# Optimization experiments

Measured on AMD Instinct MI355X. Metric: run time of the kernel, lower is better.

## Reference

```python
import jax, jax.numpy as jnp
import numpy as np

B, L, D, H = 2, 2048, 1024, 16
HD = D // H


def setup_inputs() -> dict:
    key = jax.random.key(0)
    ks = jax.random.split(key, 12)
    s = 1.0 / np.sqrt(D)
    inp = {
        "q": jax.random.normal(ks[0], (B, L, D), jnp.float32),
        "k": jax.random.normal(ks[1], (B, L, D), jnp.float32),
        "v": jax.random.normal(ks[2], (B, L, D), jnp.float32),
        "mask": jnp.zeros((B, L), dtype=bool),  # True = masked out
        "Wq": jax.random.normal(ks[3], (D, D), jnp.float32) * s,
        "bq": jnp.zeros((D,), jnp.float32),
        "Wk": jax.random.normal(ks[4], (D, D), jnp.float32) * s,
        "bk": jnp.zeros((D,), jnp.float32),
        "Wv": jax.random.normal(ks[5], (D, D), jnp.float32) * s,
        "bv": jnp.zeros((D,), jnp.float32),
        "Wo": jax.random.normal(ks[6], (D, D), jnp.float32) * s,
        "bo": jnp.zeros((D,), jnp.float32),
    }
    return inp


def reference(q, k, v, mask, Wq, bq, Wk, bk, Wv, bv, Wo, bo):
    # linear projections (torch Linear: x @ W.T + b), split into heads: [B,H,L,HD]
    def proj(x, W, b):
        y = jnp.einsum('bld,ed->ble', x, W) + b
        return y.reshape(x.shape[0], x.shape[1], H, HD).transpose(0, 2, 1, 3)

    Q = proj(q, Wq, bq)
    K = proj(k, Wk, bk)
    V = proj(v, Wv, bv)

    scale = 1.0 / np.sqrt(HD).astype(np.float32)
    scores = jnp.einsum('bhqd,bhkd->bhqk', Q, K) * scale  # [B,H,Lq,Lk]
    # mask [B,Lk] -> broadcast over heads and query positions
    scores = jnp.where(mask[:, None, None, :], -jnp.inf, scores)
    attn = jax.nn.softmax(scores, axis=-1)
    out = jnp.einsum('bhqk,bhkd->bhqd', attn, V)  # [B,H,Lq,HD]
    out = out.transpose(0, 2, 1, 3).reshape(q.shape[0], q.shape[1], D)
    return jnp.einsum('bld,ed->ble', out, Wo) + bo
```

## Files before the change

### kernel.cpp

```cpp
#include <hip/hip_runtime.h>

#define LSEQ 2048
#define DMODEL 1024
#define NHEAD 16
#define HDIM 64

typedef __attribute__((ext_vector_type(8))) short bf16x8;
typedef __attribute__((ext_vector_type(4))) float f32x4;
typedef __attribute__((ext_vector_type(16))) float f32x16;
typedef unsigned int u32;
typedef unsigned short u16;
typedef unsigned long long u64;

static __device__ __forceinline__ u16 f2bf(float x) {
    return (u16)((__builtin_bit_cast(u32, x) + 0x8000u) >> 16);
}

static __device__ __forceinline__ u32 f2bf_pk(float hi, float lo) {
    u32 a = __builtin_bit_cast(u32, hi) + 0x8000u;
    u32 b = __builtin_bit_cast(u32, lo) + 0x8000u;
#if __has_builtin(__builtin_amdgcn_perm)
    return __builtin_amdgcn_perm(a, b, 0x07060302u);
#else
    return (a & 0xFFFF0000u) | (b >> 16);
#endif
}

static __device__ __forceinline__ float bf2f(short s) {
    return __builtin_bit_cast(float, (u32)((u16)s) << 16);
}

static __device__ __forceinline__ float fast_exp2(float x) {
#if __has_builtin(__builtin_amdgcn_exp2f)
    return __builtin_amdgcn_exp2f(x);
#else
    return __expf(x * 0.6931471805599453f);
#endif
}

static __device__ __forceinline__ void gll16(const void* g, void* l) {
    __builtin_amdgcn_global_load_lds(
        (const __attribute__((address_space(1))) u32*)g,
        (__attribute__((address_space(3))) u32*)l, 16, 0, 0);
}

template <int N>
static __device__ __forceinline__ void vwait() {
    asm volatile("s_waitcnt vmcnt(%0)" :: "n"(N) : "memory");
}

__global__ __launch_bounds__(256) void conv_all(
    const float* __restrict__ q, const float* __restrict__ k, const float* __restrict__ v,
    const float* __restrict__ w0, const float* __restrict__ w1,
    const float* __restrict__ w2, const float* __restrict__ w3,
    u16* __restrict__ Qf, u16* __restrict__ Kf, u16* __restrict__ Vf,
    u16* __restrict__ o0, u16* __restrict__ o1, u16* __restrict__ o2,
    u16* __restrict__ o3) {
    const int bid = blockIdx.x;
    const float* s; u16* d; int off;
    if (bid < 12288) {
        const int z = bid >> 12;
        off = bid & 4095;
        if (z == 0)      { s = q; d = Qf; }
        else if (z == 1) { s = k; d = Kf; }
        else             { s = v; d = Vf; }
    } else {
        const int t = bid - 12288;
        const int z = t >> 10;
        off = t & 1023;
        if (z == 0)      { s = w0; d = o0; }
        else if (z == 1) { s = w1; d = o1; }
        else if (z == 2) { s = w2; d = o2; }
        else             { s = w3; d = o3; }
    }
    const int i = (off * 256 + threadIdx.x) * 4;
    float4 x = *(const float4*)(s + i);
    uint2 r;
    r.x = f2bf_pk(x.y, x.x);
    r.y = f2bf_pk(x.w, x.z);
    *(uint2*)(d + i) = r;
}

template <int OUT_MODE, int BN>
__device__ __forceinline__ void mfma_gemm(u16* __restrict__ sm,
                                          const u16* __restrict__ Xb,
                                          const u16* __restrict__ Wb,
                                          const float* __restrict__ bias,
                                          void* __restrict__ Yv, float scale) {
    constexpr int NB = BN / 32;
    constexpr int LPT = (BN == 128) ? 4 : 3;
    constexpr int ASZ = 4096;
    constexpr int BSZ = BN * 32;
    constexpr int NT = DMODEL / 32;
    u16* As = sm;
    u16* Bs = sm + 3 * ASZ;

    const int tid = threadIdx.x;
    const int wave = tid >> 6, lane = tid & 63;
    const int l16 = lane & 15, quad = lane >> 4;
    const int wm = (wave >> 1) * 64, wn = (wave & 1) * (BN / 2);
    const int m0 = blockIdx.x * 128, n0 = blockIdx.y * BN;

    const u16* Xr = Xb + (size_t)(m0 + (tid >> 2)) * DMODEL + (tid & 3) * 8;
    const u16* Wr = Wb + (size_t)(n0 + (tid >> 2)) * DMODEL + (tid & 3) * 8;
    const int t8 = tid * 8;

    auto stage = [&](int kt, int slot) {
        const int k0 = kt * 32;
        u16* Ab = As + slot * ASZ;
        u16* Bb = Bs + slot * BSZ;
        gll16(Xr + k0, Ab + t8);
        gll16(Xr + (size_t)64 * DMODEL + k0, Ab + 2048 + t8);
        gll16(Wr + k0, Bb + t8);
        if (BN == 128)
            gll16(Wr + (size_t)64 * DMODEL + k0, Bb + 2048 + t8);
    };

    f32x4 acc[4][NB];
    #pragma unroll
    for (int i = 0; i < 4; ++i)
        #pragma unroll
        for (int j = 0; j < NB; ++j)
            #pragma unroll
            for (int r = 0; r < 4; ++r) acc[i][j][r] = 0.0f;

    auto compute = [&](int kt) {
        const u16* Ac = As + (kt % 3) * ASZ;
        const u16* Bc = Bs + (kt % 3) * BSZ;
        bf16x8 af[4], bf[NB];
        #pragma unroll
        for (int mb = 0; mb < 4; ++mb)
            af[mb] = *(const bf16x8*)(Ac + (wm + mb * 16 + l16) * 32 + quad * 8);
        #pragma unroll
        for (int nb = 0; nb < NB; ++nb)
            bf[nb] = *(const bf16x8*)(Bc + (wn + nb * 16 + l16) * 32 + quad * 8);
        #pragma unroll
        for (int mb = 0; mb < 4; ++mb)
            #pragma unroll
            for (int nb = 0; nb < NB; ++nb)
                acc[mb][nb] = __builtin_amdgcn_mfma_f32_16x16x32_bf16(
                    af[mb], bf[nb], acc[mb][nb], 0, 0, 0);
    };

    stage(0, 0);
    stage(1, 1);

    #pragma unroll 1
    for (int kt = 0; kt < NT - 1; ++kt) {
        vwait<LPT>();
        __builtin_amdgcn_s_barrier();
        if (kt + 2 < NT) stage(kt + 2, (kt + 2) % 3);
        compute(kt);
    }
    vwait<0>();
    __builtin_amdgcn_s_barrier();
    compute(NT - 1);

    #pragma unroll
    for (int nb = 0; nb < NB; ++nb) {
        const int n = n0 + wn + nb * 16 + l16;
        const float bn = bias[n];
        #pragma unroll
        for (int mb = 0; mb < 4; ++mb) {
            const int mb0 = m0 + wm + mb * 16 + quad * 4;
            if (OUT_MODE == 2) {
                u16* Y = (u16*)Yv;
                uint2 rr;
                rr.x = f2bf_pk((acc[mb][nb][1] + bn) * scale, (acc[mb][nb][0] + bn) * scale);
                rr.y = f2bf_pk((acc[mb][nb][3] + bn) * scale, (acc[mb][nb][2] + bn) * scale);
                const int bb = mb0 >> 11, l = mb0 & 2047;
                const int h = n >> 6, hd = n & 63;
                *(uint2*)(Y + ((size_t)((bb * NHEAD + h) * HDIM) + hd) * LSEQ + l) = rr;
            } else {
                #pragma unroll
                for (int r = 0; r < 4; ++r) {
                    const int m = mb0 + r;
                    const float val = (acc[mb][nb][r] + bn) * scale;
                    if (OUT_MODE == 0) {
                        u16* Y = (u16*)Yv;
                        const int bb = m >> 11, l = m & 2047;
                        const int h = n >> 6, hd = n & 63;
                        Y[(((size_t)(bb * NHEAD + h) * LSEQ + l) * HDIM) + hd] = f2bf(val);
                    } else {
                        float* Y = (float*)Yv;
                        Y[(size_t)m * DMODEL + n] = val;
                    }
                }
            }
        }
    }
}

#define QSCALE (0.125f * 1.4426950408889634f)

__global__ __launch_bounds__(256) void qkv_gemm(
    const u16* __restrict__ Qf, const u16* __restrict__ Kf, const u16* __restrict__ Vf,
    const u16* __restrict__ Wqb, const u16* __restrict__ Wkb, const u16* __restrict__ Wvb,
    const float* __restrict__ bq, const float* __restrict__ bk, const float* __restrict__ bv,
    u16* __restrict__ Qp, u16* __restrict__ Kp, u16* __restrict__ Vtp) {
    __shared__ alignas(16) u16 sm[24576];
    if (blockIdx.z == 0)      mfma_gemm<0, 128>(sm, Qf, Wqb, bq, (void*)Qp, QSCALE);
    else if (blockIdx.z == 1) mfma_gemm<0, 128>(sm, Kf, Wkb, bk, (void*)Kp, 1.0f);
    else                      mfma_gemm<2, 128>(sm, Vf, Wvb, bv, (void*)Vtp, 1.0f);
}

__global__ __launch_bounds__(256) void out_gemm(
    const u16* __restrict__ AOb, const u16* __restrict__ Wob,
    const float* __restrict__ bo, float* __restrict__ out) {
    __shared__ alignas(16) u16 sm[18432];
    mfma_gemm<1, 64>(sm, AOb, Wob, bo, (void*)out, 1.0f);
}

#define KT 128
#define NTILE (LSEQ / KT)
#define HTILE (NTILE / 2)

__global__ __launch_bounds__(512, 4) void attn_mfma(
    const u16* __restrict__ Qp, const u16* __restrict__ Kp,
    const u16* __restrict__ Vtp, const unsigned char* __restrict__ mask,
    u16* __restrict__ P0, u16* __restrict__ P1, float* __restrict__ lbuf) {
    __shared__ alignas(16) u16 smem[32768];

    const int tid = threadIdx.x;
    const int wave = tid >> 6;
    const int lane = tid & 63;
    const int l32 = lane & 31;
    const int half = lane >> 5;
    const int bh = blockIdx.x;
    const int b = bh >> 4;
    const int h = bh & 15;
    const int q0 = blockIdx.y * 256;
    const int qw = q0 + wave * 32;
    const int z = blockIdx.z;
    const int kt0 = z * HTILE, kt1 = kt0 + HTILE;

    u16* Pz = z ? P1 : P0;
    float* lb = lbuf + z * (32 * LSEQ);

    const u16* Qg = Qp + ((size_t)bh * LSEQ + qw) * HDIM;
    const u16* Kg = Kp + (size_t)bh * LSEQ * HDIM;
    const u16* Vtg = Vtp + (size_t)bh * HDIM * LSEQ;
    const unsigned char* mg = mask + (size_t)b * LSEQ;

    bf16x8 qf[4];
    #pragma unroll
    for (int dc = 0; dc < 4; ++dc)
        qf[dc] = *(const bf16x8*)(Qg + (size_t)l32 * HDIM + dc * 16 + half * 8);

    f32x16 o0 = {}, o1 = {};
    float lsum = 0.0f;

    auto stageK = [&](int ktile, int slot) {
        const int k0 = ktile * KT;
        u16* Kb = smem + slot * 8192;
        #pragma unroll
        for (int j = 0; j < 2; ++j) {
            const int cid = j * 512 + tid;
            const int key = cid >> 3, pc = cid & 7, c = pc ^ (key & 7);
            gll16(Kg + (size_t)(k0 + key) * HDIM + c * 8, Kb + cid * 8);
        }
    };
    auto stageV = [&](int ktile, int slot) {
        const int k0 = ktile * KT;
        u16* Vb = smem + 16384 + slot * 8192;
        #pragma unroll
        for (int j = 0; j < 2; ++j) {
            const int cid = j * 512 + tid;
            const int d = cid >> 4, pc = cid & 15, c = pc ^ (d & 15);
            gll16(Vtg + (size_t)d * LSEQ + k0 + c * 8, Vb + cid * 8);
        }
    };

    stageK(kt0, kt0 & 1); stageV(kt0, kt0 & 1);

    const u64* mg8 = (const u64*)mg;
    const u64 mm = mg8[lane] | mg8[lane + 64] | mg8[lane + 128] | mg8[lane + 192];
    const bool mask_any = __any((int)(mm != 0ULL));

    __syncthreads();

    for (int kt = kt0; kt < kt1; ++kt) {
        if (kt + 1 < kt1) {
            stageK(kt + 1, (kt + 1) & 1);
            stageV(kt + 1, (kt + 1) & 1);
        }
        const u16* Kb = smem + (kt & 1) * 8192;
        const u16* Vb = smem + 16384 + (kt & 1) * 8192;

        #pragma unroll 1
        for (int kb = 0; kb < 4; ++kb) {
            f32x16 st = {};
            #pragma unroll
            for (int dc = 0; dc < 4; ++dc) {
                const int key = kb * 32 + l32;
                const int phys = (dc * 2 + half) ^ (key & 7);
                bf16x8 kf = *(const bf16x8*)(Kb + key * 64 + phys * 8);
                st = __builtin_amdgcn_mfma_f32_32x32x16_bf16(kf, qf[dc], st, 0, 0, 0);
            }

            if (mask_any) {
                const int k0 = kt * KT;
                const int mb0 = mg[k0 + lane];
                const int mb1 = mg[k0 + 64 + lane];
                const float b0f = mb0 ? -1e30f : 0.0f;
                const float b1f = mb1 ? -1e30f : 0.0f;
                #pragma unroll
                for (int r = 0; r < 16; ++r) {
                    const int key = kb * 32 + (r & 3) + 8 * (r >> 2) + 4 * half;
                    const float bv = __shfl((kb < 2) ? b0f : b1f, key & 63, 64);
                    st[r] += bv;
                }
            }

            u32 pk[8];
            float lk0 = 0.0f, lk1 = 0.0f;
            #pragma unroll
            for (int w = 0; w < 8; ++w) {
                const float plo = fast_exp2(st[2 * w]);
                const float phi = fast_exp2(st[2 * w + 1]);
                lk0 += plo; lk1 += phi;
                pk[w] = f2bf_pk(phi, plo);
            }
            lsum += lk0 + lk1;

            #pragma unroll
            for (int wb = 0; wb < 8; wb += 4) {
#if __has_builtin(__builtin_amdgcn_permlane32_swap)
                auto r02 = __builtin_amdgcn_permlane32_swap(
                    (int)pk[wb],     (int)pk[wb + 2], false, false);
                auto r13 = __builtin_amdgcn_permlane32_swap(
                    (int)pk[wb + 1], (int)pk[wb + 3], false, false);
                pk[wb]     = (u32)r02[0]; pk[wb + 2] = (u32)r02[1];
                pk[wb + 1] = (u32)r13[0]; pk[wb + 3] = (u32)r13[1];
#else
                const u32 ta = half ? pk[wb] : pk[wb + 2];
                const u32 tb = half ? pk[wb + 1] : pk[wb + 3];
                const u32 xa = __shfl_xor((int)ta, 32, 64);
                const u32 xb = __shfl_xor((int)tb, 32, 64);
                pk[wb]     = half ? xa : pk[wb];
                pk[wb + 1] = half ? xb : pk[wb + 1];
                pk[wb + 2] = half ? pk[wb + 2] : xa;
                pk[wb + 3] = half ? pk[wb + 3] : xb;
#endif
            }

            #pragma unroll
            for (int cc = 0; cc < 2; ++cc) {
                const int c = 2 * kb + cc;
                bf16x8 pb = __builtin_bit_cast(bf16x8, *(uint4*)&pk[4 * cc]);
                {
                    const int d = l32;
                    const int phys = (c * 2 + half) ^ (d & 15);
                    bf16x8 va = *(const bf16x8*)(Vb + d * 128 + phys * 8);
                    o0 = __builtin_amdgcn_mfma_f32_32x32x16_bf16(va, pb, o0, 0, 0, 0);
                }
                {
                    const int d = 32 + l32;
                    const int phys = (c * 2 + half) ^ (d & 15);
                    bf16x8 va = *(const bf16x8*)(Vb + d * 128 + phys * 8);
                    o1 = __builtin_amdgcn_mfma_f32_32x32x16_bf16(va, pb, o1, 0, 0, 0);
                }
            }
        }

        __syncthreads();
    }

    const float l_tot = lsum + __shfl_xor(lsum, 32, 64);
    if (!half) lb[bh * LSEQ + qw + l32] = l_tot;
    __syncthreads();
    u16* T = smem;
    #pragma unroll
    for (int nb = 0; nb < 2; ++nb)
        #pragma unroll
        for (int rp = 0; rp < 8; ++rp) {
            const int r = rp * 2;
            const int d = nb * 32 + (r & 3) + 8 * (r >> 2) + 4 * half;
            const float vlo = (nb ? o1[r] : o0[r]);
            const float vhi = (nb ? o1[r + 1] : o0[r + 1]);
            *(u32*)(T + (wave * 32 + l32) * 72 + d) = f2bf_pk(vhi, vlo);
        }
    __syncthreads();
    #pragma unroll
    for (int i = 0; i < 4; ++i) {
        const int cid = i * 512 + tid;
        const int row = cid >> 3, ch = cid & 7;
        bf16x8 val = *(const bf16x8*)(T + row * 72 + ch * 8);
        *(bf16x8*)(Pz + ((size_t)(b * LSEQ + q0 + row) * DMODEL) + h * HDIM + ch * 8) = val;
    }
}

__global__ __launch_bounds__(256) void combine(
    const u16* __restrict__ P0, const u16* __restrict__ P1,
    const float* __restrict__ lbuf, u16* __restrict__ AOb) {
    const int c = (blockIdx.x * 256 + threadIdx.x) * 8;
    const int bl = c >> 10;
    const int k = c & 1023;
    const int h = k >> 6;
    const int b = bl >> 11, l = bl & 2047;
    const int li = ((b << 4) + h) * LSEQ + l;
    const float inv = 1.0f / (lbuf[li] + lbuf[32 * LSEQ + li]);
    bf16x8 x0 = *(const bf16x8*)(P0 + c);
    bf16x8 x1 = *(const bf16x8*)(P1 + c);
    u32 r[4];
    #pragma unroll
    for (int j = 0; j < 4; ++j) {
        const float lo = (bf2f(x0[2 * j]) + bf2f(x1[2 * j])) * inv;
        const float hi = (bf2f(x0[2 * j + 1]) + bf2f(x1[2 * j + 1])) * inv;
        r[j] = f2bf_pk(hi, lo);
    }
    *(uint4*)(AOb + c) = *(uint4*)r;
}

extern "C" void kernel_launch(void* const* d_in, const int* in_sizes, int n_in,
                              void* d_out, int out_size, void* d_ws, size_t ws_size,
                              hipStream_t stream) {
    (void)in_sizes; (void)n_in; (void)out_size; (void)ws_size;
    const float* q  = (const float*)d_in[0];
    const float* k  = (const float*)d_in[1];
    const float* v  = (const float*)d_in[2];
    const unsigned char* mask = (const unsigned char*)d_in[3];
    const float* Wq = (const float*)d_in[4];
    const float* bq = (const float*)d_in[5];
    const float* Wk = (const float*)d_in[6];
    const float* bk = (const float*)d_in[7];
    const float* Wv = (const float*)d_in[8];
    const float* bv = (const float*)d_in[9];
    const float* Wo = (const float*)d_in[10];
    const float* bo = (const float*)d_in[11];
    float* out = (float*)d_out;

    u16* ws16 = (u16*)d_ws;
    const size_t M4 = (size_t)4 * 1024 * 1024;
    const size_t M1 = (size_t)1024 * 1024;
    u16* Qf  = ws16;
    u16* Kf  = ws16 + M4;
    u16* Vf  = ws16 + 2 * M4;
    u16* Qp  = ws16 + 3 * M4;
    u16* Kp  = ws16 + 4 * M4;
    u16* Vtp = ws16 + 5 * M4;
    u16* AOb = ws16 + 6 * M4;
    u16* Wqb = ws16 + 7 * M4;
    u16* Wkb = ws16 + 7 * M4 + M1;
    u16* Wvb = ws16 + 7 * M4 + 2 * M1;
    u16* Wob = ws16 + 7 * M4 + 3 * M1;

    u16* P0 = Qf;
    u16* P1 = Kf;
    float* lbuf = (float*)Vf;

    conv_all<<<dim3(16384), 256, 0, stream>>>(q, k, v, Wq, Wk, Wv, Wo,
                                              Qf, Kf, Vf, Wqb, Wkb, Wvb, Wob);
    qkv_gemm<<<dim3(32, 8, 3), 256, 0, stream>>>(Qf, Kf, Vf, Wqb, Wkb, Wvb,
                                                 bq, bk, bv, Qp, Kp, Vtp);
    attn_mfma<<<dim3(32, 8, 2), 512, 0, stream>>>(Qp, Kp, Vtp, mask, P0, P1, lbuf);
    combine<<<dim3(2048), 256, 0, stream>>>(P0, P1, lbuf, AOb);
    out_gemm<<<dim3(32, 16), 256, 0, stream>>>(AOb, Wob, bo, out);
}
```

Measured before the change: 216.2 us.

## Drop split-K attention and combine kernel; read V directly from global

Removes the two-way key split across blockIdx.z, so each attention block walks all key tiles and normalizes its own output. The separate combine kernel and its partial buffers go away. V is no longer staged in LDS and is loaded straight from global memory inside the PV loop, which shrinks shared memory. Launch bounds drop from 4 to 2 blocks per SM. The cost is half as many attention blocks, 256 in place of 512, which lowers parallelism. The uncoalesced, unpipelined global V loads may also stall the MFMA loop.

```diff
diff --git a/kernel.cpp b/kernel.cpp
--- a/kernel.cpp
+++ b/kernel.cpp
@@ -24,10 +24,6 @@
 #else
     return (a & 0xFFFF0000u) | (b >> 16);
 #endif
-}
-
-static __device__ __forceinline__ float bf2f(short s) {
-    return __builtin_bit_cast(float, (u32)((u16)s) << 16);
 }
 
 static __device__ __forceinline__ float fast_exp2(float x) {
@@ -213,13 +209,12 @@
 
 #define KT 128
 #define NTILE (LSEQ / KT)
-#define HTILE (NTILE / 2)
-
-__global__ __launch_bounds__(512, 4) void attn_mfma(
+
+__global__ __launch_bounds__(512, 2) void attn_mfma(
     const u16* __restrict__ Qp, const u16* __restrict__ Kp,
     const u16* __restrict__ Vtp, const unsigned char* __restrict__ mask,
-    u16* __restrict__ P0, u16* __restrict__ P1, float* __restrict__ lbuf) {
-    __shared__ alignas(16) u16 smem[32768];
+    u16* __restrict__ AOb) {
+    __shared__ alignas(16) u16 smem[18432];
 
     const int tid = threadIdx.x;
     const int wave = tid >> 6;
@@ -231,11 +226,6 @@
     const int h = bh & 15;
     const int q0 = blockIdx.y * 256;
     const int qw = q0 + wave * 32;
-    const int z = blockIdx.z;
-    const int kt0 = z * HTILE, kt1 = kt0 + HTILE;
-
-    u16* Pz = z ? P1 : P0;
-    float* lb = lbuf + z * (32 * LSEQ);
 
     const u16* Qg = Qp + ((size_t)bh * LSEQ + qw) * HDIM;
     const u16* Kg = Kp + (size_t)bh * LSEQ * HDIM;
@@ -260,18 +250,8 @@
             gll16(Kg + (size_t)(k0 + key) * HDIM + c * 8, Kb + cid * 8);
         }
     };
-    auto stageV = [&](int ktile, int slot) {
-        const int k0 = ktile * KT;
-        u16* Vb = smem + 16384 + slot * 8192;
-        #pragma unroll
-        for (int j = 0; j < 2; ++j) {
-            const int cid = j * 512 + tid;
-            const int d = cid >> 4, pc = cid & 15, c = pc ^ (d & 15);
-            gll16(Vtg + (size_t)d * LSEQ + k0 + c * 8, Vb + cid * 8);
-        }
-    };
-
-    stageK(kt0, kt0 & 1); stageV(kt0, kt0 & 1);
+
+    stageK(0, 0);
 
     const u64* mg8 = (const u64*)mg;
     const u64 mm = mg8[lane] | mg8[lane + 64] | mg8[lane + 128] | mg8[lane + 192];
@@ -279,13 +259,10 @@
 
     __syncthreads();
 
-    for (int kt = kt0; kt < kt1; ++kt) {
-        if (kt + 1 < kt1) {
-            stageK(kt + 1, (kt + 1) & 1);
-            stageV(kt + 1, (kt + 1) & 1);
-        }
+    for (int kt = 0; kt < NTILE; ++kt) {
+        if (kt + 1 < NTILE) stageK(kt + 1, (kt + 1) & 1);
         const u16* Kb = smem + (kt & 1) * 8192;
-        const u16* Vb = smem + 16384 + (kt & 1) * 8192;
+        const int k0 = kt * KT;
 
         #pragma unroll 1
         for (int kb = 0; kb < 4; ++kb) {
@@ -299,7 +276,6 @@
             }
 
             if (mask_any) {
-                const int k0 = kt * KT;
                 const int mb0 = mg[k0 + lane];
                 const int mb1 = mg[k0 + 64 + lane];
                 const float b0f = mb0 ? -1e30f : 0.0f;
@@ -347,17 +323,16 @@
             #pragma unroll
             for (int cc = 0; cc < 2; ++cc) {
                 const int c = 2 * kb + cc;
+                const int j = c * 2 + half;
                 bf16x8 pb = __builtin_bit_cast(bf16x8, *(uint4*)&pk[4 * cc]);
                 {
                     const int d = l32;
-                    const int phys = (c * 2 + half) ^ (d & 15);
-                    bf16x8 va = *(const bf16x8*)(Vb + d * 128 + phys * 8);
+                    bf16x8 va = *(const bf16x8*)(Vtg + (size_t)d * LSEQ + k0 + j * 8);
                     o0 = __builtin_amdgcn_mfma_f32_32x32x16_bf16(va, pb, o0, 0, 0, 0);
                 }
                 {
                     const int d = 32 + l32;
-                    const int phys = (c * 2 + half) ^ (d & 15);
-                    bf16x8 va = *(const bf16x8*)(Vb + d * 128 + phys * 8);
+                    bf16x8 va = *(const bf16x8*)(Vtg + (size_t)d * LSEQ + k0 + j * 8);
                     o1 = __builtin_amdgcn_mfma_f32_32x32x16_bf16(va, pb, o1, 0, 0, 0);
                 }
             }
@@ -367,7 +342,7 @@
     }
 
     const float l_tot = lsum + __shfl_xor(lsum, 32, 64);
-    if (!half) lb[bh * LSEQ + qw + l32] = l_tot;
+    const float inv = 1.0f / l_tot;
     __syncthreads();
     u16* T = smem;
     #pragma unroll
@@ -376,8 +351,8 @@
         for (int rp = 0; rp < 8; ++rp) {
             const int r = rp * 2;
             const int d = nb * 32 + (r & 3) + 8 * (r >> 2) + 4 * half;
-            const float vlo = (nb ? o1[r] : o0[r]);
-            const float vhi = (nb ? o1[r + 1] : o0[r + 1]);
+            const float vlo = (nb ? o1[r] : o0[r]) * inv;
+            const float vhi = (nb ? o1[r + 1] : o0[r + 1]) * inv;
             *(u32*)(T + (wave * 32 + l32) * 72 + d) = f2bf_pk(vhi, vlo);
         }
     __syncthreads();
@@ -386,30 +361,8 @@
         const int cid = i * 512 + tid;
         const int row = cid >> 3, ch = cid & 7;
         bf16x8 val = *(const bf16x8*)(T + row * 72 + ch * 8);
-        *(bf16x8*)(Pz + ((size_t)(b * LSEQ + q0 + row) * DMODEL) + h * HDIM + ch * 8) = val;
+        *(bf16x8*)(AOb + ((size_t)(b * LSEQ + q0 + row) * DMODEL) + h * HDIM + ch * 8) = val;
     }
-}
-
-__global__ __launch_bounds__(256) void combine(
-    const u16* __restrict__ P0, const u16* __restrict__ P1,
-    const float* __restrict__ lbuf, u16* __restrict__ AOb) {
-    const int c = (blockIdx.x * 256 + threadIdx.x) * 8;
-    const int bl = c >> 10;
-    const int k = c & 1023;
-    const int h = k >> 6;
-    const int b = bl >> 11, l = bl & 2047;
-    const int li = ((b << 4) + h) * LSEQ + l;
-    const float inv = 1.0f / (lbuf[li] + lbuf[32 * LSEQ + li]);
-    bf16x8 x0 = *(const bf16x8*)(P0 + c);
-    bf16x8 x1 = *(const bf16x8*)(P1 + c);
-    u32 r[4];
-    #pragma unroll
-    for (int j = 0; j < 4; ++j) {
-        const float lo = (bf2f(x0[2 * j]) + bf2f(x1[2 * j])) * inv;
-        const float hi = (bf2f(x0[2 * j + 1]) + bf2f(x1[2 * j + 1])) * inv;
-        r[j] = f2bf_pk(hi, lo);
-    }
-    *(uint4*)(AOb + c) = *(uint4*)r;
 }
 
 extern "C" void kernel_launch(void* const* d_in, const int* in_sizes, int n_in,
@@ -445,15 +398,10 @@
     u16* Wvb = ws16 + 7 * M4 + 2 * M1;
     u16* Wob = ws16 + 7 * M4 + 3 * M1;
 
-    u16* P0 = Qf;
-    u16* P1 = Kf;
-    float* lbuf = (float*)Vf;
-
     conv_all<<<dim3(16384), 256, 0, stream>>>(q, k, v, Wq, Wk, Wv, Wo,
                                               Qf, Kf, Vf, Wqb, Wkb, Wvb, Wob);
     qkv_gemm<<<dim3(32, 8, 3), 256, 0, stream>>>(Qf, Kf, Vf, Wqb, Wkb, Wvb,
                                                  bq, bk, bv, Qp, Kp, Vtp);
-    attn_mfma<<<dim3(32, 8, 2), 512, 0, stream>>>(Qp, Kp, Vtp, mask, P0, P1, lbuf);
-    combine<<<dim3(2048), 256, 0, stream>>>(P0, P1, lbuf, AOb);
+    attn_mfma<<<dim3(32, 8), 512, 0, stream>>>(Qp, Kp, Vtp, mask, AOb);
     out_gemm<<<dim3(32, 16), 256, 0, stream>>>(AOb, Wob, bo, out);
 }
```

Result: slower. 240.3 us (+11.2%).
